# Kernel tuning notes

Hardware: AMD Instinct MI355X
Metric: run time of the kernel (lower is better)

Reference implementation:

```python
import jax, jax.numpy as jnp
import numpy as np
import math

EMB = 1024
HEADS = 16
B, S = 2, 2048


def setup_inputs() -> dict:
    key = jax.random.key(0)
    k_x, k_wq, k_bq, k_wu, k_bu = jax.random.split(key, 5)
    lim = 1.0 / math.sqrt(EMB)
    x = jax.random.normal(k_x, (B, S, EMB), dtype=jnp.float32)
    # nn.Linear weights: [out, in], uniform(-lim, lim)
    wq = jax.random.uniform(k_wq, (EMB, EMB), jnp.float32, -lim, lim)
    bq = jax.random.uniform(k_bq, (EMB,), jnp.float32, -lim, lim)
    wu = jax.random.uniform(k_wu, (EMB, EMB), jnp.float32, -lim, lim)
    bu = jax.random.uniform(k_bu, (EMB,), jnp.float32, -lim, lim)
    return {"x": x, "wq": wq, "bq": bq, "wu": wu, "bu": bu}


def reference(x, wq, bq, wu, bu):
    b, s, emb = x.shape
    hd = emb // HEADS
    # NOTE: faithful to the original bug — Q, K, V all come from toqueries
    q = jnp.einsum('bse,oe->bso', x, wq) + bq  # [B,S,emb]
    # faithful (buggy) reshape: heads in LEADING dim
    qh = q.reshape(HEADS, b, s, hd)
    kh = qh
    vh = qh
    scale = 1.0 / math.sqrt(emb)  # faithful: sqrt(emb), not sqrt(hd)
    scores = jnp.einsum('hbqd,hbkd->hbqk', qh, kh) * scale  # [H,B,S,S]
    attn = jax.nn.softmax(scores, axis=-1)
    out = jnp.einsum('hbqk,hbkd->hbqd', attn, vh)  # [H,B,S,hd]
    out = out.reshape(b, s, emb)
    return jnp.einsum('bse,oe->bso', out, wu) + bu
```

## Files before the change

kernel.cpp:

```cpp
#include <hip/hip_runtime.h>
#include <stdint.h>

#define EMB 1024
#define HEADS 16
#define NB 2
#define NS 2048
#define HD 64
#define NTOK (NB*NS)
#define KVBLK 64
#define SEXP2 0.04508421676368185f

typedef __attribute__((ext_vector_type(8))) short short8;
typedef __attribute__((ext_vector_type(4))) float f32x4;
typedef __attribute__((ext_vector_type(4))) unsigned int u32x4;

__device__ inline unsigned short f2bf(float f) {
  unsigned int x = __builtin_bit_cast(unsigned int, f);
  x += 0x7FFFu + ((x >> 16) & 1u);
  return (unsigned short)(x >> 16);
}

__device__ inline unsigned cvt_pk_bf16(float lo, float hi) {
  unsigned d;
  asm("v_cvt_pk_bf16_f32 %0, %1, %2" : "=v"(d) : "v"(lo), "v"(hi));
  return d;
}

__device__ inline void gld16(const void* g, void* l) {
  __builtin_amdgcn_global_load_lds(
      (const __attribute__((address_space(1))) unsigned int*)g,
      (__attribute__((address_space(3))) unsigned int*)l, 16, 0, 0);
}

__global__ void cvt_bf16_kernel(const float* __restrict__ s,
                                unsigned short* __restrict__ d, int n) {
  int i = (blockIdx.x * blockDim.x + threadIdx.x) * 8;
  if (i >= n) return;
  float4 v0 = *reinterpret_cast<const float4*>(s + i);
  float4 v1 = *reinterpret_cast<const float4*>(s + i + 4);
  short8 o;
  o[0] = (short)f2bf(v0.x); o[1] = (short)f2bf(v0.y);
  o[2] = (short)f2bf(v0.z); o[3] = (short)f2bf(v0.w);
  o[4] = (short)f2bf(v1.x); o[5] = (short)f2bf(v1.y);
  o[6] = (short)f2bf(v1.z); o[7] = (short)f2bf(v1.w);
  *reinterpret_cast<short8*>(d + i) = o;
}

__global__ void cvt_bf16x2_kernel(const float* __restrict__ s0,
                                  unsigned short* __restrict__ d0,
                                  const float* __restrict__ s1,
                                  unsigned short* __restrict__ d1, int n0, int n1) {
  int i = (blockIdx.x * blockDim.x + threadIdx.x) * 8;
  const float* s; unsigned short* d;
  if (i < n0) { s = s0 + i; d = d0 + i; }
  else if (i - n0 < n1) { s = s1 + (i - n0); d = d1 + (i - n0); }
  else return;
  float4 v0 = *reinterpret_cast<const float4*>(s);
  float4 v1 = *reinterpret_cast<const float4*>(s + 4);
  short8 o;
  o[0] = (short)f2bf(v0.x); o[1] = (short)f2bf(v0.y);
  o[2] = (short)f2bf(v0.z); o[3] = (short)f2bf(v0.w);
  o[4] = (short)f2bf(v1.x); o[5] = (short)f2bf(v1.y);
  o[6] = (short)f2bf(v1.z); o[7] = (short)f2bf(v1.w);
  *reinterpret_cast<short8*>(d) = o;
}

__global__ __launch_bounds__(256) void transpose_kernel(
    const unsigned short* __restrict__ src, unsigned short* __restrict__ dst) {
  __shared__ unsigned short t[64][72];
  const int slab = blockIdx.y, kt = blockIdx.x;
  const unsigned short* s = src + ((size_t)slab * NS + kt * 64) * HD;
  unsigned short* d = dst + (size_t)slab * HD * NS + kt * 64;
  const int tid = threadIdx.x;
  #pragma unroll
  for (int c = 0; c < 2; ++c) {
    int idx = c * 256 + tid;
    int row = idx >> 3, col = (idx & 7) * 8;
    short8 v = *reinterpret_cast<const short8*>(s + row * HD + col);
    *reinterpret_cast<short8*>(&t[row][col]) = v;
  }
  __syncthreads();
  #pragma unroll
  for (int c = 0; c < 2; ++c) {
    int idx = c * 256 + tid;
    int drow = idx >> 3, col = (idx & 7) * 8;
    short8 v;
    #pragma unroll
    for (int j = 0; j < 8; ++j) {
      int p = col + j;
      int kv = (p & 32) | (((p >> 2) & 1) << 4) | (((p >> 3) & 3) << 2) | (p & 3);
      v[j] = t[kv][drow];
    }
    *reinterpret_cast<short8*>(d + (size_t)drow * NS + col) = v;
  }
}

template<bool OUT_BF16>
__global__ __launch_bounds__(256) void gemm_bt_kernel(
    const unsigned short* __restrict__ A,
    const unsigned short* __restrict__ Bw,
    const float* __restrict__ bias,
    void* __restrict__ Cout,
    unsigned short* __restrict__ Qscaled,
    int M, int N, int K) {
  __shared__ __align__(16) unsigned short As[2][64 * 64];
  __shared__ __align__(16) unsigned short Bs[2][64 * 64];
  const int tid = threadIdx.x;
  const int lane = tid & 63;
  const int wave = tid >> 6;
  const int wr = wave >> 1, wc = wave & 1;
  const int g = lane >> 4, r = lane & 15;
  const int brow = blockIdx.y * 64;
  const int bcol = blockIdx.x * 64;

  const f32x4 zf = {0.f, 0.f, 0.f, 0.f};
  f32x4 acc[2][2];
  #pragma unroll
  for (int m = 0; m < 2; ++m)
    #pragma unroll
    for (int n = 0; n < 2; ++n) acc[m][n] = zf;

  auto stage = [&](int bb, int k0) {
    #pragma unroll
    for (int i = 0; i < 2; ++i) {
      int base = i * 4096 + wave * 1024;
      int L = base + lane * 16;
      int row = L >> 7, lsl = ((L >> 4) & 7) ^ (row & 7);
      gld16((const char*)A + ((size_t)(brow + row) * K + k0) * 2 + lsl * 16,
            (char*)&As[bb][0] + base);
    }
    #pragma unroll
    for (int i = 0; i < 2; ++i) {
      int base = i * 4096 + wave * 1024;
      int L = base + lane * 16;
      int row = L >> 7, lsl = ((L >> 4) & 7) ^ (row & 7);
      gld16((const char*)Bw + ((size_t)(bcol + row) * K + k0) * 2 + lsl * 16,
            (char*)&Bs[bb][0] + base);
    }
  };

  stage(0, 0);
  int cur = 0;
  for (int k0 = 0; k0 < K; k0 += 64) {
    __syncthreads();
    if (k0 + 64 < K) stage(cur ^ 1, k0 + 64);
    const char* Ac = (const char*)&As[cur][0];
    const char* Bc = (const char*)&Bs[cur][0];
    short8 af[2][2], bfr[2][2];
    #pragma unroll
    for (int m = 0; m < 2; ++m) {
      int row = wr * 32 + m * 16 + r;
      #pragma unroll
      for (int kk = 0; kk < 2; ++kk)
        af[m][kk] = *reinterpret_cast<const short8*>(
            Ac + row * 128 + ((kk * 64 + g * 16) ^ ((row & 7) << 4)));
    }
    #pragma unroll
    for (int n = 0; n < 2; ++n) {
      int row = wc * 32 + n * 16 + r;
      #pragma unroll
      for (int kk = 0; kk < 2; ++kk)
        bfr[n][kk] = *reinterpret_cast<const short8*>(
            Bc + row * 128 + ((kk * 64 + g * 16) ^ ((row & 7) << 4)));
    }
    #pragma unroll
    for (int kk = 0; kk < 2; ++kk)
      #pragma unroll
      for (int m = 0; m < 2; ++m)
        #pragma unroll
        for (int n = 0; n < 2; ++n)
          acc[m][n] = __builtin_amdgcn_mfma_f32_16x16x32_bf16(af[m][kk], bfr[n][kk], acc[m][n], 0, 0, 0);
    cur ^= 1;
  }

  #pragma unroll
  for (int n = 0; n < 2; ++n) {
    int col = bcol + wc * 32 + n * 16 + r;
    float bv = bias[col];
    #pragma unroll
    for (int m = 0; m < 2; ++m) {
      #pragma unroll
      for (int reg = 0; reg < 4; ++reg) {
        int row = brow + wr * 32 + m * 16 + g * 4 + reg;
        float v = acc[m][n][reg] + bv;
        if (OUT_BF16)
          ((unsigned short*)Cout)[(size_t)row * N + col] = f2bf(v);
        else
          ((float*)Cout)[(size_t)row * N + col] = v;
        if (Qscaled)
          Qscaled[(size_t)row * N + col] = f2bf(v * SEXP2);
      }
    }
  }
}

__global__ __launch_bounds__(128) void attn_kernel(
    const unsigned short* __restrict__ qb,
    const unsigned short* __restrict__ qsb,
    const unsigned short* __restrict__ vtb,
    unsigned short* __restrict__ ob) {
  const int bid = blockIdx.x;
  const int xcd = bid & 7, idx = bid >> 3;
  const int slab = xcd * 4 + (idx >> 5);
  const int qtile = idx & 31;
  const unsigned short* Qs = qb + (size_t)slab * NS * HD;
  const unsigned short* Qss = qsb + (size_t)slab * NS * HD;
  const unsigned short* Vts = vtb + (size_t)slab * HD * NS;
  unsigned short* Os = ob + (size_t)slab * NS * HD;
  const int tid = threadIdx.x;
  const int lane = tid & 63;
  const int wave = tid >> 6;
  const int g = lane >> 4, r = lane & 15;
  const int qrow0 = qtile * 64 + wave * 32;
  const int rkey = (r & 7) << 4;

  __shared__ __align__(16) unsigned short K_lds[2][KVBLK * HD];
  __shared__ __align__(16) unsigned short Vt_lds[2][HD * KVBLK];

  auto stage = [&](int bb, int kt) {
    const char* Kg = (const char*)(Qs + (size_t)kt * KVBLK * HD);
    const char* Vg = (const char*)Vts + (size_t)kt * 128;
    #pragma unroll
    for (int i = 0; i < 4; ++i) {
      int base = (i * 2 + wave) * 1024;
      int L = base + lane * 16;
      int row = L >> 7, lsl = ((L >> 4) & 7) ^ (row & 7);
      gld16(Kg + row * 128 + lsl * 16, (char*)&K_lds[bb][0] + base);
      gld16(Vg + (size_t)row * (NS * 2) + lsl * 16, (char*)&Vt_lds[bb][0] + base);
    }
  };

  short8 aq[2][2];
  #pragma unroll
  for (int m = 0; m < 2; ++m)
    #pragma unroll
    for (int kk = 0; kk < 2; ++kk)
      aq[m][kk] = *reinterpret_cast<const short8*>(
          &Qss[(size_t)(qrow0 + m * 16 + r) * HD + kk * 32 + g * 8]);
  asm volatile("s_waitcnt vmcnt(0)" ::: "memory");

  const f32x4 zf = {0.f, 0.f, 0.f, 0.f};
  f32x4 o_acc[2][4];
  float l_lane[2] = {0.f, 0.f};
  #pragma unroll
  for (int m = 0; m < 2; ++m)
    #pragma unroll
    for (int n = 0; n < 4; ++n) o_acc[m][n] = zf;

  stage(0, 0);
  int cur = 0;
  for (int kt = 0; kt < NS / KVBLK; ++kt) {
    __builtin_amdgcn_s_barrier();
    if (kt + 1 < NS / KVBLK) {
      stage(cur ^ 1, kt + 1);
      asm volatile("s_waitcnt vmcnt(8)" ::: "memory");
    } else {
      asm volatile("s_waitcnt vmcnt(0)" ::: "memory");
    }
    __builtin_amdgcn_s_barrier();
    __builtin_amdgcn_sched_barrier(0);

    const char* Kc = (const char*)&K_lds[cur][0];
    const char* Vc = (const char*)&Vt_lds[cur][0];

    f32x4 s[2][4];
    #pragma unroll
    for (int jb = 0; jb < 4; ++jb) {
      short8 bk[2];
      #pragma unroll
      for (int kk = 0; kk < 2; ++kk)
        bk[kk] = *reinterpret_cast<const short8*>(
            Kc + (jb * 16 + r) * 128 + ((kk * 64 + g * 16) ^ rkey));
      #pragma unroll
      for (int m = 0; m < 2; ++m) {
        s[m][jb] = zf;
        #pragma unroll
        for (int kk = 0; kk < 2; ++kk)
          s[m][jb] = __builtin_amdgcn_mfma_f32_16x16x32_bf16(bk[kk], aq[m][kk], s[m][jb], 0, 0, 0);
      }
    }

    short8 ap[2][2];
    #pragma unroll
    for (int m = 0; m < 2; ++m) {
      float p[4][4];
      #pragma unroll
      for (int jb = 0; jb < 4; ++jb)
        #pragma unroll
        for (int reg = 0; reg < 4; ++reg)
          p[jb][reg] = __builtin_amdgcn_exp2f(s[m][jb][reg]);
      float t0 = (p[0][0] + p[0][1]) + (p[0][2] + p[0][3]);
      float t1 = (p[1][0] + p[1][1]) + (p[1][2] + p[1][3]);
      float t2 = (p[2][0] + p[2][1]) + (p[2][2] + p[2][3]);
      float t3 = (p[3][0] + p[3][1]) + (p[3][2] + p[3][3]);
      l_lane[m] += (t0 + t1) + (t2 + t3);
      #pragma unroll
      for (int kk = 0; kk < 2; ++kk) {
        u32x4 w;
        w.x = cvt_pk_bf16(p[2 * kk][0], p[2 * kk][1]);
        w.y = cvt_pk_bf16(p[2 * kk][2], p[2 * kk][3]);
        w.z = cvt_pk_bf16(p[2 * kk + 1][0], p[2 * kk + 1][1]);
        w.w = cvt_pk_bf16(p[2 * kk + 1][2], p[2 * kk + 1][3]);
        ap[m][kk] = __builtin_bit_cast(short8, w);
      }
    }

    #pragma unroll
    for (int n = 0; n < 4; ++n) {
      short8 bv[2];
      #pragma unroll
      for (int kk = 0; kk < 2; ++kk)
        bv[kk] = *reinterpret_cast<const short8*>(
            Vc + (n * 16 + r) * 128 + ((kk * 64 + g * 16) ^ rkey));
      #pragma unroll
      for (int m = 0; m < 2; ++m)
        #pragma unroll
        for (int kk = 0; kk < 2; ++kk)
          o_acc[m][n] = __builtin_amdgcn_mfma_f32_16x16x32_bf16(ap[m][kk], bv[kk], o_acc[m][n], 0, 0, 0);
    }
    cur ^= 1;
  }

  #pragma unroll
  for (int m = 0; m < 2; ++m) {
    float l = l_lane[m];
    l += __shfl_xor(l, 16);
    l += __shfl_xor(l, 32);
    #pragma unroll
    for (int reg = 0; reg < 4; ++reg) {
      float inv = 1.f / __shfl(l, g * 4 + reg);
      int row = qrow0 + m * 16 + g * 4 + reg;
      #pragma unroll
      for (int n = 0; n < 4; ++n)
        Os[(size_t)row * HD + n * 16 + r] = f2bf(o_acc[m][n][reg] * inv);
    }
  }
}

extern "C" void kernel_launch(void* const* d_in, const int* in_sizes, int n_in,
                              void* d_out, int out_size, void* d_ws, size_t ws_size,
                              hipStream_t stream) {
  const float* x  = (const float*)d_in[0];
  const float* wq = (const float*)d_in[1];
  const float* bq = (const float*)d_in[2];
  const float* wu = (const float*)d_in[3];
  const float* bu = (const float*)d_in[4];
  float* out = (float*)d_out;

  char* ws = (char*)d_ws;
  unsigned short* xb  = (unsigned short*)(ws);
  unsigned short* qb  = (unsigned short*)(ws + (8u  << 20));
  unsigned short* ob  = (unsigned short*)(ws + (16u << 20));
  unsigned short* wqb = (unsigned short*)(ws + (24u << 20));
  unsigned short* wub = (unsigned short*)(ws + (26u << 20));

  cvt_bf16_kernel<<<(NTOK * EMB / 8 + 255) / 256, 256, 0, stream>>>(x, xb, NTOK * EMB);
  cvt_bf16x2_kernel<<<(2 * EMB * EMB / 8 + 255) / 256, 256, 0, stream>>>(
      wq, wqb, wu, wub, EMB * EMB, EMB * EMB);

  unsigned short* qsb = ob;
  gemm_bt_kernel<true><<<dim3(EMB / 64, NTOK / 64), 256, 0, stream>>>(
      xb, wqb, bq, qb, qsb, NTOK, EMB, EMB);

  unsigned short* vtb = xb;
  transpose_kernel<<<dim3(NS / 64, HEADS * NB), 256, 0, stream>>>(qb, vtb);

  attn_kernel<<<dim3(1024), 128, 0, stream>>>(qb, qsb, vtb, ob);

  gemm_bt_kernel<false><<<dim3(EMB / 64, NTOK / 64), 256, 0, stream>>>(
      ob, wub, bu, out, (unsigned short*)nullptr, NTOK, EMB, EMB);
}
```

Baseline: 107.4 us.

## Split attention KV loop across wave pairs with LDS reduction; merge convert kernels

```diff
diff --git a/kernel.cpp b/kernel.cpp
--- a/kernel.cpp
+++ b/kernel.cpp
@@ -32,28 +32,17 @@
       (__attribute__((address_space(3))) unsigned int*)l, 16, 0, 0);
 }
 
-__global__ void cvt_bf16_kernel(const float* __restrict__ s,
-                                unsigned short* __restrict__ d, int n) {
-  int i = (blockIdx.x * blockDim.x + threadIdx.x) * 8;
-  if (i >= n) return;
-  float4 v0 = *reinterpret_cast<const float4*>(s + i);
-  float4 v1 = *reinterpret_cast<const float4*>(s + i + 4);
-  short8 o;
-  o[0] = (short)f2bf(v0.x); o[1] = (short)f2bf(v0.y);
-  o[2] = (short)f2bf(v0.z); o[3] = (short)f2bf(v0.w);
-  o[4] = (short)f2bf(v1.x); o[5] = (short)f2bf(v1.y);
-  o[6] = (short)f2bf(v1.z); o[7] = (short)f2bf(v1.w);
-  *reinterpret_cast<short8*>(d + i) = o;
-}
-
-__global__ void cvt_bf16x2_kernel(const float* __restrict__ s0,
-                                  unsigned short* __restrict__ d0,
+__global__ void cvt_bf16x3_kernel(const float* __restrict__ s0,
+                                  unsigned short* __restrict__ d0, int n0,
                                   const float* __restrict__ s1,
-                                  unsigned short* __restrict__ d1, int n0, int n1) {
+                                  unsigned short* __restrict__ d1, int n1,
+                                  const float* __restrict__ s2,
+                                  unsigned short* __restrict__ d2, int n2) {
   int i = (blockIdx.x * blockDim.x + threadIdx.x) * 8;
   const float* s; unsigned short* d;
   if (i < n0) { s = s0 + i; d = d0 + i; }
   else if (i - n0 < n1) { s = s1 + (i - n0); d = d1 + (i - n0); }
+  else if (i - n0 - n1 < n2) { s = s2 + (i - n0 - n1); d = d2 + (i - n0 - n1); }
   else return;
   float4 v0 = *reinterpret_cast<const float4*>(s);
   float4 v1 = *reinterpret_cast<const float4*>(s + 4);
@@ -194,15 +183,15 @@
   }
 }
 
-__global__ __launch_bounds__(128) void attn_kernel(
+__global__ __launch_bounds__(512) void attn_kernel(
     const unsigned short* __restrict__ qb,
     const unsigned short* __restrict__ qsb,
     const unsigned short* __restrict__ vtb,
     unsigned short* __restrict__ ob) {
   const int bid = blockIdx.x;
   const int xcd = bid & 7, idx = bid >> 3;
-  const int slab = xcd * 4 + (idx >> 5);
-  const int qtile = idx & 31;
+  const int slab = xcd * 4 + (idx >> 4);
+  const int qtile = idx & 15;
   const unsigned short* Qs = qb + (size_t)slab * NS * HD;
   const unsigned short* Qss = qsb + (size_t)slab * NS * HD;
   const unsigned short* Vts = vtb + (size_t)slab * HD * NS;
@@ -210,23 +199,26 @@
   const int tid = threadIdx.x;
   const int lane = tid & 63;
   const int wave = tid >> 6;
+  const int qsub = wave >> 1;
+  const int h = wave & 1;
   const int g = lane >> 4, r = lane & 15;
-  const int qrow0 = qtile * 64 + wave * 32;
+  const int qrow0 = qtile * 128 + qsub * 32;
   const int rkey = (r & 7) << 4;
 
-  __shared__ __align__(16) unsigned short K_lds[2][KVBLK * HD];
-  __shared__ __align__(16) unsigned short Vt_lds[2][HD * KVBLK];
-
-  auto stage = [&](int bb, int kt) {
-    const char* Kg = (const char*)(Qs + (size_t)kt * KVBLK * HD);
-    const char* Vg = (const char*)Vts + (size_t)kt * 128;
-    #pragma unroll
-    for (int i = 0; i < 4; ++i) {
-      int base = (i * 2 + wave) * 1024;
+  __shared__ __align__(16) unsigned short K_lds[2][2][KVBLK * HD];
+  __shared__ __align__(16) unsigned short Vt_lds[2][2][HD * KVBLK];
+
+  auto stage = [&](int bb, int t) {
+    int kt2 = 2 * t + h;
+    const char* Kg = (const char*)Qs + (size_t)kt2 * 8192;
+    const char* Vg = (const char*)Vts + (size_t)kt2 * 128;
+    #pragma unroll
+    for (int i = 0; i < 2; ++i) {
+      int base = (qsub * 2 + i) * 1024;
       int L = base + lane * 16;
       int row = L >> 7, lsl = ((L >> 4) & 7) ^ (row & 7);
-      gld16(Kg + row * 128 + lsl * 16, (char*)&K_lds[bb][0] + base);
-      gld16(Vg + (size_t)row * (NS * 2) + lsl * 16, (char*)&Vt_lds[bb][0] + base);
+      gld16(Kg + row * 128 + lsl * 16, (char*)&K_lds[h][bb][0] + base);
+      gld16(Vg + (size_t)row * (NS * 2) + lsl * 16, (char*)&Vt_lds[h][bb][0] + base);
     }
   };
 
@@ -237,7 +229,6 @@
     for (int kk = 0; kk < 2; ++kk)
       aq[m][kk] = *reinterpret_cast<const short8*>(
           &Qss[(size_t)(qrow0 + m * 16 + r) * HD + kk * 32 + g * 8]);
-  asm volatile("s_waitcnt vmcnt(0)" ::: "memory");
 
   const f32x4 zf = {0.f, 0.f, 0.f, 0.f};
   f32x4 o_acc[2][4];
@@ -249,19 +240,11 @@
 
   stage(0, 0);
   int cur = 0;
-  for (int kt = 0; kt < NS / KVBLK; ++kt) {
-    __builtin_amdgcn_s_barrier();
-    if (kt + 1 < NS / KVBLK) {
-      stage(cur ^ 1, kt + 1);
-      asm volatile("s_waitcnt vmcnt(8)" ::: "memory");
-    } else {
-      asm volatile("s_waitcnt vmcnt(0)" ::: "memory");
-    }
-    __builtin_amdgcn_s_barrier();
-    __builtin_amdgcn_sched_barrier(0);
-
-    const char* Kc = (const char*)&K_lds[cur][0];
-    const char* Vc = (const char*)&Vt_lds[cur][0];
+  for (int t = 0; t < NS / KVBLK / 2; ++t) {
+    __syncthreads();
+    if (t + 1 < NS / KVBLK / 2) stage(cur ^ 1, t + 1);
+    const char* Kc = (const char*)&K_lds[h][cur][0];
+    const char* Vc = (const char*)&Vt_lds[h][cur][0];
 
     f32x4 s[2][4];
     #pragma unroll
@@ -321,18 +304,42 @@
     cur ^= 1;
   }
 
-  #pragma unroll
-  for (int m = 0; m < 2; ++m) {
-    float l = l_lane[m];
-    l += __shfl_xor(l, 16);
-    l += __shfl_xor(l, 32);
-    #pragma unroll
-    for (int reg = 0; reg < 4; ++reg) {
-      float inv = 1.f / __shfl(l, g * 4 + reg);
-      int row = qrow0 + m * 16 + g * 4 + reg;
+  __syncthreads();
+  char* redO = (char*)&K_lds[0][0][0];
+  char* redL = (char*)&Vt_lds[0][0][0];
+  if (h == 1) {
+    #pragma unroll
+    for (int m = 0; m < 2; ++m)
       #pragma unroll
       for (int n = 0; n < 4; ++n)
-        Os[(size_t)row * HD + n * 16 + r] = f2bf(o_acc[m][n][reg] * inv);
+        *reinterpret_cast<f32x4*>(redO + qsub * 8192 + (m * 4 + n) * 1024 + lane * 16) = o_acc[m][n];
+    float2 lp; lp.x = l_lane[0]; lp.y = l_lane[1];
+    *reinterpret_cast<float2*>(redL + qsub * 512 + lane * 8) = lp;
+  }
+  __syncthreads();
+  if (h == 0) {
+    #pragma unroll
+    for (int m = 0; m < 2; ++m)
+      #pragma unroll
+      for (int n = 0; n < 4; ++n)
+        o_acc[m][n] += *reinterpret_cast<f32x4*>(
+            redO + qsub * 8192 + (m * 4 + n) * 1024 + lane * 16);
+    float2 lp = *reinterpret_cast<float2*>(redL + qsub * 512 + lane * 8);
+    l_lane[0] += lp.x; l_lane[1] += lp.y;
+
+    #pragma unroll
+    for (int m = 0; m < 2; ++m) {
+      float l = l_lane[m];
+      l += __shfl_xor(l, 16);
+      l += __shfl_xor(l, 32);
+      #pragma unroll
+      for (int reg = 0; reg < 4; ++reg) {
+        float inv = 1.f / __shfl(l, g * 4 + reg);
+        int row = qrow0 + m * 16 + g * 4 + reg;
+        #pragma unroll
+        for (int n = 0; n < 4; ++n)
+          Os[(size_t)row * HD + n * 16 + r] = f2bf(o_acc[m][n][reg] * inv);
+      }
     }
   }
 }
@@ -354,9 +361,9 @@
   unsigned short* wqb = (unsigned short*)(ws + (24u << 20));
   unsigned short* wub = (unsigned short*)(ws + (26u << 20));
 
-  cvt_bf16_kernel<<<(NTOK * EMB / 8 + 255) / 256, 256, 0, stream>>>(x, xb, NTOK * EMB);
-  cvt_bf16x2_kernel<<<(2 * EMB * EMB / 8 + 255) / 256, 256, 0, stream>>>(
-      wq, wqb, wu, wub, EMB * EMB, EMB * EMB);
+  const int nx = NTOK * EMB, nw = EMB * EMB;
+  cvt_bf16x3_kernel<<<((nx + 2 * nw) / 8 + 255) / 256, 256, 0, stream>>>(
+      x, xb, nx, wq, wqb, nw, wu, wub, nw);
 
   unsigned short* qsb = ob;
   gemm_bt_kernel<true><<<dim3(EMB / 64, NTOK / 64), 256, 0, stream>>>(
@@ -365,7 +372,7 @@
   unsigned short* vtb = xb;
   transpose_kernel<<<dim3(NS / 64, HEADS * NB), 256, 0, stream>>>(qb, vtb);
 
-  attn_kernel<<<dim3(1024), 128, 0, stream>>>(qb, qsb, vtb, ob);
+  attn_kernel<<<dim3(512), 512, 0, stream>>>(qb, qsb, vtb, ob);
 
   gemm_bt_kernel<false><<<dim3(EMB / 64, NTOK / 64), 256, 0, stream>>>(
       ob, wub, bu, out, (unsigned short*)nullptr, NTOK, EMB, EMB);
```

Result: faster. 91.26 us (-15.0%).
